# Kernel optimization log

Hardware: AMD Instinct MI355X
Metric: run time of the kernel (lower is better)

Reference implementation:

```python
import jax, jax.numpy as jnp
import numpy as np

B, S, K, N = 2, 2048, 4096, 16384

def setup_inputs() -> dict:
    key = jax.random.key(0)
    k1, k2, k3, k4 = jax.random.split(key, 4)
    x = jax.random.normal(k1, (B, S, K), dtype=jnp.float32)
    # int8-valued quantized weight stored as int32 for portability
    weight_q = jax.random.randint(k2, (N, K), -127, 128, dtype=jnp.int32)
    scale = jax.random.uniform(k3, (1,), dtype=jnp.float32, minval=0.01, maxval=0.05)
    bias = jax.random.normal(k4, (N,), dtype=jnp.float32)
    return {"x": x, "weight_q": weight_q, "scale": scale, "bias": bias}

def reference(x, weight_q, scale, bias):
    # Dequantize int8 weight with per-tensor symmetric scale, then column-parallel matmul.
    w = weight_q.astype(x.dtype) * scale  # [N, K]
    y = jnp.einsum('bsk,nk->bsn', x, w) + bias  # [B, S, N]
    return y
```

## Files before the change

### kernel.cpp

```cpp
#include <hip/hip_runtime.h>
#include <stdint.h>
#include <stddef.h>


#define M_TOT 4096
#define N_TOT 16384
#define K_TOT 4096
#define NT    64

typedef __attribute__((ext_vector_type(4))) int      v4i;
typedef __attribute__((ext_vector_type(8))) _Float16 f16x8;
typedef __attribute__((ext_vector_type(4))) float    f32x4;

#define GLOAD_LDS16(g, l) __builtin_amdgcn_global_load_lds(                  \
    (const __attribute__((address_space(1))) void*)(g),                      \
    (__attribute__((address_space(3))) void*)(l), 16, 0, 0)


__global__ __launch_bounds__(256) void cvt_x_i8(const float* __restrict__ x,
                                                signed char* __restrict__ o,
                                                float* __restrict__ sx) {
  const int row = blockIdx.x;
  const int tid = threadIdx.x;
  const float* xr = x + (size_t)row * K_TOT;
  float4 v[4];
  float mx = 0.f;
#pragma unroll
  for (int j = 0; j < 4; ++j) {
    v[j] = ((const float4*)xr)[tid * 4 + j];
    mx = fmaxf(mx, fmaxf(fmaxf(fabsf(v[j].x), fabsf(v[j].y)),
                         fmaxf(fabsf(v[j].z), fabsf(v[j].w))));
  }
#pragma unroll
  for (int off = 32; off; off >>= 1) mx = fmaxf(mx, __shfl_xor(mx, off));
  __shared__ float wm[4];
  if ((tid & 63) == 0) wm[tid >> 6] = mx;
  __syncthreads();
  const float m4 = fmaxf(fmaxf(wm[0], wm[1]), fmaxf(wm[2], wm[3]));
  const float smax = fmaxf(m4, 1e-6f);
  const float inv  = 127.0f / smax;
  if (tid == 0) sx[row] = smax / 127.0f;
  int p[4];
#pragma unroll
  for (int j = 0; j < 4; ++j) {
    int q0 = (int)rintf(v[j].x * inv), q1 = (int)rintf(v[j].y * inv);
    int q2 = (int)rintf(v[j].z * inv), q3 = (int)rintf(v[j].w * inv);
    q0 = max(-127, min(127, q0)); q1 = max(-127, min(127, q1));
    q2 = max(-127, min(127, q2)); q3 = max(-127, min(127, q3));
    p[j] = (q0 & 255) | ((q1 & 255) << 8) | ((q2 & 255) << 16) | (q3 << 24);
  }
  ((int4*)(o + (size_t)row * K_TOT))[tid] = make_int4(p[0], p[1], p[2], p[3]);
}

__global__ __launch_bounds__(256) void cvt_w_i8(const int* __restrict__ w,
                                                signed char* __restrict__ o, int n16) {
  const int stride = gridDim.x * blockDim.x;
  for (int i = blockIdx.x * blockDim.x + threadIdx.x; i < n16; i += stride) {
    int p[4];
#pragma unroll
    for (int j = 0; j < 4; ++j) {
      int4 a = ((const int4*)w)[i * 4 + j];
      p[j] = (a.x & 255) | ((a.y & 255) << 8) | ((a.z & 255) << 16) | (a.w << 24);
    }
    ((int4*)o)[i] = make_int4(p[0], p[1], p[2], p[3]);
  }
}


__device__ __forceinline__ void stage_i8(const signed char* __restrict__ g,
                                         size_t kbyte, signed char* l, int tid) {
#pragma unroll
  for (int j = 0; j < 2; ++j) {
    const int ci  = j * 512 + tid;
    const int row = ci >> 2;
    const int sc  = (ci & 3) ^ ((row >> 1) & 3);
    GLOAD_LDS16(g + (size_t)row * K_TOT + kbyte + sc * 16, l + ci * 16);
  }
}

__device__ __forceinline__ v4i fragi(const signed char* region, int r, int hi) {
  return *(const v4i*)(region + r * 64 + ((hi ^ ((r >> 1) & 3)) << 4));
}

#define BAR()  do { __builtin_amdgcn_s_barrier(); \
                    __builtin_amdgcn_sched_barrier(0); } while (0)

#define READ_FRAGS(A, B, At, Bt)                                              \
  do {                                                                        \
    _Pragma("unroll")                                                         \
    for (int m = 0; m < 8; ++m) A[m] = fragi(At, wr * 128 + m * 16 + lr, hi); \
    _Pragma("unroll")                                                         \
    for (int n = 0; n < 4; ++n) B[n] = fragi(Bt, wc * 64 + n * 16 + lr, hi);  \
  } while (0)

#define MFMA_TILE(A, B)                                                       \
  do {                                                                        \
    _Pragma("unroll")                                                         \
    for (int m = 0; m < 8; ++m)                                               \
      _Pragma("unroll")                                                       \
      for (int n = 0; n < 4; ++n)                                             \
        acc[m][n] = __builtin_amdgcn_mfma_i32_16x16x64_i8(A[m], B[n],         \
                                                          acc[m][n], 0, 0, 0);\
  } while (0)

__global__ __launch_bounds__(512, 2) void gemm_i8(
    const signed char* __restrict__ A8, const signed char* __restrict__ B8,
    const float* __restrict__ sx, const float* __restrict__ scale_p,
    const float* __restrict__ bias, float* __restrict__ out)
{
  __shared__ __align__(16) signed char lds[4][2][16384];

  const int tid  = threadIdx.x;
  const int lane = tid & 63;
  const int wave = tid >> 6;
  const int wr = wave >> 2;
  const int wc = wave & 3;
  const int lr = lane & 15;
  const int hi = lane >> 4;

  const int bid = blockIdx.x;
  const int wg  = (bid & 7) * 128 + (bid >> 3);
  const int bm  = wg & 15;
  const int bn  = wg >> 4;
  const int arow0 = bm * 256;
  const int brow0 = bn * 256;

  const signed char* Ag = A8 + (size_t)arow0 * K_TOT;
  const signed char* Bg = B8 + (size_t)brow0 * K_TOT;

  v4i acc[8][4];
#pragma unroll
  for (int m = 0; m < 8; ++m)
#pragma unroll
    for (int n = 0; n < 4; ++n)
      acc[m][n] = (v4i){0, 0, 0, 0};

  stage_i8(Ag, 0,   &lds[0][0][0], tid);
  stage_i8(Bg, 0,   &lds[0][1][0], tid);
  stage_i8(Ag, 64,  &lds[1][0][0], tid);
  stage_i8(Bg, 64,  &lds[1][1][0], tid);
  stage_i8(Ag, 128, &lds[2][0][0], tid);
  stage_i8(Bg, 128, &lds[2][1][0], tid);
  asm volatile("s_waitcnt vmcnt(4)" ::: "memory");
  BAR();

  v4i a0[8], b0[4], a1[8], b1[4];
  READ_FRAGS(a0, b0, &lds[0][0][0], &lds[0][1][0]);

  for (int t = 0; t < NT; t += 2) {
    {
      if (t + 3 < NT) {
        const size_t k3 = (size_t)(t + 3) * 64;
        stage_i8(Ag, k3, &lds[(t + 3) & 3][0][0], tid);
        stage_i8(Bg, k3, &lds[(t + 3) & 3][1][0], tid);
      }
      const signed char* At1 = &lds[(t + 1) & 3][0][0];
      const signed char* Bt1 = &lds[(t + 1) & 3][1][0];
      READ_FRAGS(a1, b1, At1, Bt1);
      MFMA_TILE(a0, b0);
      if (t + 3 < NT) asm volatile("s_waitcnt vmcnt(4)" ::: "memory");
      else            asm volatile("s_waitcnt vmcnt(0)" ::: "memory");
      BAR();
    }
    {
      if (t + 4 < NT) {
        const size_t k4 = (size_t)(t + 4) * 64;
        stage_i8(Ag, k4, &lds[(t + 4) & 3][0][0], tid);
        stage_i8(Bg, k4, &lds[(t + 4) & 3][1][0], tid);
      }
      if (t + 2 < NT) {
        const signed char* At2 = &lds[(t + 2) & 3][0][0];
        const signed char* Bt2 = &lds[(t + 2) & 3][1][0];
        READ_FRAGS(a0, b0, At2, Bt2);
      }
      MFMA_TILE(a1, b1);
      if (t + 4 < NT) asm volatile("s_waitcnt vmcnt(4)" ::: "memory");
      else            asm volatile("s_waitcnt vmcnt(0)" ::: "memory");
      BAR();
    }
  }

  const float s = scale_p[0];
  float bv[4];
#pragma unroll
  for (int n = 0; n < 4; ++n) bv[n] = bias[brow0 + wc * 64 + n * 16 + lr];
#pragma unroll
  for (int mi = 0; mi < 8; ++mi) {
    const int row0 = arow0 + wr * 128 + (mi >> 2) * 64 + (mi & 3) * 16 + hi * 4;
    float sc4[4];
#pragma unroll
    for (int j = 0; j < 4; ++j) sc4[j] = sx[row0 + j] * s;
#pragma unroll
    for (int n = 0; n < 4; ++n) {
      const int col = brow0 + wc * 64 + n * 16 + lr;
      const v4i v = acc[mi][n];
#pragma unroll
      for (int j = 0; j < 4; ++j)
        out[(size_t)(row0 + j) * N_TOT + col] = (float)v[j] * sc4[j] + bv[n];
    }
  }
}


__global__ __launch_bounds__(256) void gemm_direct(
    const float* __restrict__ Xf, const int* __restrict__ Wq,
    const float* __restrict__ scale_p, const float* __restrict__ bias,
    float* __restrict__ out)
{
  __shared__ _Float16 ldsA[128 * 64];
  __shared__ _Float16 ldsB[128 * 64];
  const int tid = threadIdx.x, lane = tid & 63, wave = tid >> 6;
  const int wr = wave >> 1, wc = wave & 1;
  const int bid = blockIdx.x;
  const int wg  = (bid & 7) * 512 + (bid >> 3);
  const int arow0 = (wg & 31) * 128, brow0 = (wg >> 5) * 128;
  f32x4 acc[4][4];
#pragma unroll
  for (int m = 0; m < 4; ++m)
#pragma unroll
    for (int n = 0; n < 4; ++n) acc[m][n] = (f32x4){0.f, 0.f, 0.f, 0.f};
  const int srow = tid >> 3, schunk = tid & 7;
  const int lr = lane & 15, hi = lane >> 4;
  for (int kt = 0; kt < K_TOT / 64; ++kt) {
    const size_t kbase = (size_t)kt * 64;
    __syncthreads();
#pragma unroll
    for (int i = 0; i < 4; ++i) {
      const int row = i * 32 + srow;
      const int p = schunk ^ (row & 7);
      const float* gx = Xf + (size_t)(arow0 + row) * K_TOT + kbase + schunk * 8;
      const int*   gw = Wq + (size_t)(brow0 + row) * K_TOT + kbase + schunk * 8;
      float4 x0 = ((const float4*)gx)[0];
      float4 x1 = ((const float4*)gx)[1];
      int4   w0 = ((const int4*)gw)[0];
      int4   w1 = ((const int4*)gw)[1];
      f16x8 ha = { (_Float16)x0.x, (_Float16)x0.y, (_Float16)x0.z, (_Float16)x0.w,
                   (_Float16)x1.x, (_Float16)x1.y, (_Float16)x1.z, (_Float16)x1.w };
      f16x8 hb = { (_Float16)w0.x, (_Float16)w0.y, (_Float16)w0.z, (_Float16)w0.w,
                   (_Float16)w1.x, (_Float16)w1.y, (_Float16)w1.z, (_Float16)w1.w };
      *(f16x8*)(ldsA + row * 64 + p * 8) = ha;
      *(f16x8*)(ldsB + row * 64 + p * 8) = hb;
    }
    __syncthreads();
#pragma unroll
    for (int s2 = 0; s2 < 2; ++s2) {
      f16x8 af2[4], bf2[4];
#pragma unroll
      for (int m = 0; m < 4; ++m) {
        const int r = wr * 64 + m * 16 + lr;
        af2[m] = *(const f16x8*)(ldsA + r * 64 + (((s2 * 4 + hi) ^ (r & 7)) * 8));
      }
#pragma unroll
      for (int n = 0; n < 4; ++n) {
        const int r = wc * 64 + n * 16 + lr;
        bf2[n] = *(const f16x8*)(ldsB + r * 64 + (((s2 * 4 + hi) ^ (r & 7)) * 8));
      }
#pragma unroll
      for (int m = 0; m < 4; ++m)
#pragma unroll
        for (int n = 0; n < 4; ++n)
          acc[m][n] = __builtin_amdgcn_mfma_f32_16x16x32_f16(af2[m], bf2[n], acc[m][n], 0, 0, 0);
    }
  }
  const float s = scale_p[0];
#pragma unroll
  for (int n = 0; n < 4; ++n) {
    const int col = brow0 + wc * 64 + n * 16 + lr;
    const float bvv = bias[col];
#pragma unroll
    for (int m = 0; m < 4; ++m) {
      const int row0 = arow0 + wr * 64 + m * 16 + hi * 4;
      const f32x4 v = acc[m][n];
#pragma unroll
      for (int j = 0; j < 4; ++j)
        out[(size_t)(row0 + j) * N_TOT + col] = v[j] * s + bvv;
    }
  }
}


extern "C" void kernel_launch(void* const* d_in, const int* in_sizes, int n_in,
                              void* d_out, int out_size, void* d_ws, size_t ws_size,
                              hipStream_t stream) {
  const float* x     = (const float*)d_in[0];
  const int*   wq    = (const int*)d_in[1];
  const float* scale = (const float*)d_in[2];
  const float* bias  = (const float*)d_in[3];
  float*       out   = (float*)d_out;

  const size_t nA = (size_t)M_TOT * K_TOT;
  const size_t nB = (size_t)N_TOT * K_TOT;
  const size_t need = nA + nB + M_TOT * sizeof(float);

  if (ws_size >= need) {
    signed char* A8 = (signed char*)d_ws;
    signed char* B8 = A8 + nA;
    float*       sx = (float*)(B8 + nB);
    cvt_x_i8<<<M_TOT, 256, 0, stream>>>(x, A8, sx);
    cvt_w_i8<<<2048, 256, 0, stream>>>(wq, B8, (int)(nB / 16));
    gemm_i8<<<(M_TOT / 256) * (N_TOT / 256), 512, 0, stream>>>(A8, B8, sx, scale, bias, out);
  } else {
    gemm_direct<<<(M_TOT / 128) * (N_TOT / 128), 256, 0, stream>>>(x, wq, scale, bias, out);
  }
}
```

Measured before the change: 417.4 us.

## Load B fragments directly from global into registers, bypassing LDS

Weight (B) fragments are now read by each wave straight from global memory into registers one k-step ahead. Only the activation (A) tile is staged through LDS, which halves the LDS footprint and drops the B LDS reads and their bank swizzle. Sched-group barriers are also added inside the MFMA loop to interleave LDS reads, global loads and MFMAs. In exchange, the two wave rows sharing a B tile each fetch it separately, which doubles B global/L2 traffic. The loads use a narrow per-lane access pattern, and the per-iteration vmcnt wait can expose global latency with only one step of prefetch.

```diff
diff --git a/kernel.cpp b/kernel.cpp
--- a/kernel.cpp
+++ b/kernel.cpp
@@ -85,22 +85,31 @@
 #define BAR()  do { __builtin_amdgcn_s_barrier(); \
                     __builtin_amdgcn_sched_barrier(0); } while (0)
 
-#define READ_FRAGS(A, B, At, Bt)                                              \
+#define LOAD_B(B, Bw, kb)                                                     \
+  do {                                                                        \
+    _Pragma("unroll")                                                         \
+    for (int n = 0; n < 4; ++n)                                               \
+      B[n] = *(const v4i*)((Bw) + (size_t)n * 16 * K_TOT + (kb));             \
+  } while (0)
+
+#define READ_A(A, At)                                                         \
   do {                                                                        \
     _Pragma("unroll")                                                         \
     for (int m = 0; m < 8; ++m) A[m] = fragi(At, wr * 128 + m * 16 + lr, hi); \
-    _Pragma("unroll")                                                         \
-    for (int n = 0; n < 4; ++n) B[n] = fragi(Bt, wc * 64 + n * 16 + lr, hi);  \
   } while (0)
 
 #define MFMA_TILE(A, B)                                                       \
   do {                                                                        \
     _Pragma("unroll")                                                         \
-    for (int m = 0; m < 8; ++m)                                               \
+    for (int m = 0; m < 8; ++m) {                                             \
+      __builtin_amdgcn_sched_group_barrier(0x30, 1, 0);                       \
+      __builtin_amdgcn_sched_group_barrier(0x100, 1, 0);                      \
+      __builtin_amdgcn_sched_group_barrier(0x8, 4, 0);                        \
       _Pragma("unroll")                                                       \
       for (int n = 0; n < 4; ++n)                                             \
         acc[m][n] = __builtin_amdgcn_mfma_i32_16x16x64_i8(A[m], B[n],         \
                                                           acc[m][n], 0, 0, 0);\
+    }                                                                         \
   } while (0)
 
 __global__ __launch_bounds__(512, 2) void gemm_i8(
@@ -108,7 +117,7 @@
     const float* __restrict__ sx, const float* __restrict__ scale_p,
     const float* __restrict__ bias, float* __restrict__ out)
 {
-  __shared__ __align__(16) signed char lds[4][2][16384];
+  __shared__ __align__(16) signed char lds[4][16384];
 
   const int tid  = threadIdx.x;
   const int lane = tid & 63;
@@ -126,7 +135,7 @@
   const int brow0 = bn * 256;
 
   const signed char* Ag = A8 + (size_t)arow0 * K_TOT;
-  const signed char* Bg = B8 + (size_t)brow0 * K_TOT;
+  const signed char* Bw = B8 + (size_t)(brow0 + wc * 64 + lr) * K_TOT + hi * 16;
 
   v4i acc[8][4];
 #pragma unroll
@@ -135,46 +144,32 @@
     for (int n = 0; n < 4; ++n)
       acc[m][n] = (v4i){0, 0, 0, 0};
 
-  stage_i8(Ag, 0,   &lds[0][0][0], tid);
-  stage_i8(Bg, 0,   &lds[0][1][0], tid);
-  stage_i8(Ag, 64,  &lds[1][0][0], tid);
-  stage_i8(Bg, 64,  &lds[1][1][0], tid);
-  stage_i8(Ag, 128, &lds[2][0][0], tid);
-  stage_i8(Bg, 128, &lds[2][1][0], tid);
-  asm volatile("s_waitcnt vmcnt(4)" ::: "memory");
+  v4i afA[8], afB[8], bA[4], bB[4];
+
+  LOAD_B(bA, Bw, 0);
+  stage_i8(Ag, 0,   &lds[0][0], tid);
+  stage_i8(Ag, 64,  &lds[1][0], tid);
+  stage_i8(Ag, 128, &lds[2][0], tid);
+  asm volatile("s_waitcnt vmcnt(2)" ::: "memory");
   BAR();
-
-  v4i a0[8], b0[4], a1[8], b1[4];
-  READ_FRAGS(a0, b0, &lds[0][0][0], &lds[0][1][0]);
+  READ_A(afA, &lds[0][0]);
 
   for (int t = 0; t < NT; t += 2) {
     {
-      if (t + 3 < NT) {
-        const size_t k3 = (size_t)(t + 3) * 64;
-        stage_i8(Ag, k3, &lds[(t + 3) & 3][0][0], tid);
-        stage_i8(Bg, k3, &lds[(t + 3) & 3][1][0], tid);
-      }
-      const signed char* At1 = &lds[(t + 1) & 3][0][0];
-      const signed char* Bt1 = &lds[(t + 1) & 3][1][0];
-      READ_FRAGS(a1, b1, At1, Bt1);
-      MFMA_TILE(a0, b0);
-      if (t + 3 < NT) asm volatile("s_waitcnt vmcnt(4)" ::: "memory");
+      if (t + 1 < NT) LOAD_B(bB, Bw, (size_t)(t + 1) * 64);
+      if (t + 3 < NT) stage_i8(Ag, (size_t)(t + 3) * 64, &lds[(t + 3) & 3][0], tid);
+      if (t + 1 < NT) READ_A(afB, &lds[(t + 1) & 3][0]);
+      MFMA_TILE(afA, bA);
+      if (t + 3 < NT) asm volatile("s_waitcnt vmcnt(2)" ::: "memory");
       else            asm volatile("s_waitcnt vmcnt(0)" ::: "memory");
       BAR();
     }
     {
-      if (t + 4 < NT) {
-        const size_t k4 = (size_t)(t + 4) * 64;
-        stage_i8(Ag, k4, &lds[(t + 4) & 3][0][0], tid);
-        stage_i8(Bg, k4, &lds[(t + 4) & 3][1][0], tid);
-      }
-      if (t + 2 < NT) {
-        const signed char* At2 = &lds[(t + 2) & 3][0][0];
-        const signed char* Bt2 = &lds[(t + 2) & 3][1][0];
-        READ_FRAGS(a0, b0, At2, Bt2);
-      }
-      MFMA_TILE(a1, b1);
-      if (t + 4 < NT) asm volatile("s_waitcnt vmcnt(4)" ::: "memory");
+      if (t + 2 < NT) LOAD_B(bA, Bw, (size_t)(t + 2) * 64);
+      if (t + 4 < NT) stage_i8(Ag, (size_t)(t + 4) * 64, &lds[(t + 4) & 3][0], tid);
+      if (t + 2 < NT) READ_A(afA, &lds[(t + 2) & 3][0]);
+      MFMA_TILE(afB, bB);
+      if (t + 4 < NT) asm volatile("s_waitcnt vmcnt(2)" ::: "memory");
       else            asm volatile("s_waitcnt vmcnt(0)" ::: "memory");
       BAR();
     }
```

After: 557.2 us. +33.5%, slower.
